# Optimization experiments

Measured on AMD Instinct MI355X. Metric: run time of the kernel, lower is better.

## Reference

```python
import jax, jax.numpy as jnp
import numpy as np

# ---- static synthetic forest: 64 complete binary trees, depth 9 (heap layout) ----
DEPTH = 9
N_TREES = 64
C = 8
M = 256
N_GEN = 8
NPT = 2 ** (DEPTH + 1) - 1          # 1023 nodes per tree
DIM = N_TREES * NPT                  # 65472 total nodes
_base = np.arange(N_TREES) * NPT

def _lvl_nodes(l):
    return (_base[:, None] + np.arange(2 ** l - 1, 2 ** (l + 1) - 1)[None, :]).reshape(-1)

LEVELS = []   # list of (parent_idx, child_idx) edge arrays, top level first
UPAR = []     # unique parents per level (== nodes of level l-1)
for _l in range(1, DEPTH + 1):
    _ch = np.arange(2 ** _l - 1, 2 ** (_l + 1) - 1)
    _pa = (_ch - 1) // 2
    LEVELS.append((jnp.asarray((_base[:, None] + _pa[None, :]).reshape(-1)),
                   jnp.asarray((_base[:, None] + _ch[None, :]).reshape(-1))))
    UPAR.append(jnp.asarray(_lvl_nodes(_l - 1)))
LEAVES = jnp.asarray(_lvl_nodes(DEPTH))
ROOTS = jnp.asarray(_base)
INTERNAL = jnp.asarray(np.concatenate([_lvl_nodes(l) for l in range(DEPTH)]))
TREES_IND = jnp.asarray(np.repeat(np.arange(N_TREES), NPT))
N_CH = 2.0  # every internal node has exactly 2 children -> segment mean = sum/2


def _forward(A, B, Pi, x):
    # softmax reparameterization (per generative head)
    sm_A = jax.nn.softmax(A, axis=0)          # (C,C,G), softmax over parent-state dim 0
    sm_B = jax.nn.softmax(B, axis=1)          # (C,M,G), softmax over symbols
    sm_Pi = jax.nn.softmax(Pi, axis=0)        # (C,G)

    # B[:, x] gathered per node, as (node, C, G)
    B_x = jnp.transpose(sm_B[:, x], (1, 0, 2))  # (DIM,C,G)

    # ---- reversed upward (leaves -> roots) ----
    beta = jnp.zeros((DIM, C, N_GEN), dtype=A.dtype)
    t_beta = jnp.zeros((DIM, C, N_GEN), dtype=A.dtype)
    b_leaf = sm_Pi[None, :, :] * B_x[LEAVES]                 # (L,C,G)
    beta = beta.at[LEAVES].set(b_leaf / b_leaf.sum(1, keepdims=True))
    for (pa, ch), upar in zip(reversed(LEVELS), reversed(UPAR)):
        beta_ch = beta[ch]                                   # (E,C,G)
        t_beta_ch = jnp.einsum('ijg,ejg->eig', sm_A, beta_ch)
        t_beta = t_beta + jax.ops.segment_sum(t_beta_ch, pa, num_segments=DIM) / N_CH
        beta_l = t_beta[upar] * B_x[upar]                    # (U,C,G)
        beta = beta.at[upar].set(beta_l / beta_l.sum(1, keepdims=True))

    # ---- reversed downward (roots -> leaves) ----
    eps = jnp.zeros((DIM, C, N_GEN), dtype=A.dtype)
    t_eps = jnp.zeros((DIM, C, C, N_GEN), dtype=A.dtype)
    eps = eps.at[ROOTS].set(beta[ROOTS])
    for pa, ch in LEVELS:
        # (E,Cpa,Cch,G)
        eps_joint = (eps[pa][:, :, None, :] * sm_A[None]
                     * beta[ch][:, None, :, :] / t_beta[pa][:, :, None, :])
        t_eps = t_eps + jax.ops.segment_sum(eps_joint, pa, num_segments=DIM) / N_CH
        eps = eps.at[ch].set(eps_joint.sum(1))

    # ---- log-likelihood ----
    lik = jnp.zeros((DIM, N_GEN), dtype=A.dtype)
    lik = lik.at[INTERNAL].add((t_eps[INTERNAL] * jnp.log(sm_A)[None]).sum((1, 2)))
    lik = lik + (eps * jnp.log(B_x)).sum(1)  # all_nodes == all nodes here
    lik = lik.at[LEAVES].add((eps[LEAVES] * jnp.log(sm_Pi)[None]).sum(1))
    ll = jax.ops.segment_sum(lik, TREES_IND, num_segments=N_TREES)  # (n_trees,G)
    return -ll


def setup_inputs() -> dict:
    key = jax.random.key(0)
    k1, k2, k3, k4 = jax.random.split(key, 4)
    A = jax.random.uniform(k1, (C, C, N_GEN), minval=-5.0, maxval=5.0)
    B = jax.random.uniform(k2, (C, M, N_GEN), minval=-5.0, maxval=5.0)
    Pi = jax.random.uniform(k3, (C, N_GEN), minval=-5.0, maxval=5.0)
    x = jax.random.randint(k4, (DIM,), 0, M)
    return {"A": A, "B": B, "Pi": Pi, "x": x}


def reference(A, B, Pi, x):
    return _forward(A, B, Pi, x)
```

## Files before the change

### kernel.cpp

```cpp
#include <hip/hip_runtime.h>
#include <hip/hip_bf16.h>

#define NTHREADS 256

namespace {
constexpr int C = 8;
constexpr int G = 8;
constexpr int M = 256;
constexpr int DEPTH = 9;
constexpr int NPT = 1023;
constexpr int NINT = 511;

__global__ __launch_bounds__(NTHREADS, 2)
void htmm_fused(const float* __restrict__ A, const float* __restrict__ Bm,
                const float* __restrict__ Pi, const int* __restrict__ x,
                float* __restrict__ out)
{
    __shared__ float beta[NPT][9];
    __shared__ float tbeta[NINT][9];
    __shared__ __hip_bfloat16 bx[NPT][C];
    __shared__ float smA[C][C];
    __shared__ float AlogA[C][C];
    __shared__ float smPi[C];
    __shared__ float logPi[C];
    __shared__ float den[C];
    __shared__ float part[C][32];
    __shared__ float red[NTHREADS / 64];

    const int tid  = threadIdx.x;
    const int tree = blockIdx.x >> 3;
    const int g    = blockIdx.x & 7;

    if (tid < C * C) {
        int i = tid >> 3, j = tid & 7;
        smA[i][j] = A[(i * C + j) * G + g];
    }
    {
        int i = tid >> 5, t = tid & 31;
        float s = 0.f;
        for (int m = t; m < M; m += 32)
            s += __expf(Bm[(i * M + m) * G + g]);
        part[i][t] = s;
    }
    __syncthreads();

    if (tid < C) {
        int j = tid;
        float mx = -1e30f;
        for (int i = 0; i < C; ++i) mx = fmaxf(mx, smA[i][j]);
        float s = 0.f;
        for (int i = 0; i < C; ++i) s += __expf(smA[i][j] - mx);
        float ls = __logf(s);
        float inv = 1.f / s;
        for (int i = 0; i < C; ++i) {
            float raw = smA[i][j];
            float v = __expf(raw - mx) * inv;
            smA[i][j]  = v;
            AlogA[i][j] = v * (raw - mx - ls);
        }
    } else if (tid < 2 * C) {
        int i = tid - C;
        float s = 0.f;
        for (int t = 0; t < 32; ++t) s += part[i][t];
        den[i] = s;
    } else if (tid == 2 * C) {
        float raw[C];
        float mx = -1e30f;
        for (int i = 0; i < C; ++i) { raw[i] = Pi[i * G + g]; mx = fmaxf(mx, raw[i]); }
        float s = 0.f;
        for (int i = 0; i < C; ++i) s += __expf(raw[i] - mx);
        float ls = __logf(s);
        float inv = 1.f / s;
        for (int i = 0; i < C; ++i) {
            smPi[i]  = __expf(raw[i] - mx) * inv;
            logPi[i] = raw[i] - mx - ls;
        }
    }
    __syncthreads();

    for (int n = tid; n < NPT; n += NTHREADS) {
        int xn = x[tree * NPT + n];
        #pragma unroll
        for (int i = 0; i < C; ++i) {
            float v = __expf(Bm[(i * M + xn) * G + g]) / den[i];
            bx[n][i] = __float2bfloat16(v);
        }
    }
    __syncthreads();

    for (int n0 = tid; n0 < 512; n0 += NTHREADS) {
        int n = NINT + n0;
        float b[C], s = 0.f;
        #pragma unroll
        for (int i = 0; i < C; ++i) { b[i] = smPi[i] * __bfloat162float(bx[n][i]); s += b[i]; }
        float inv = 1.f / s;
        #pragma unroll
        for (int i = 0; i < C; ++i) beta[n][i] = b[i] * inv;
    }
    __syncthreads();

    for (int l = DEPTH; l >= 1; --l) {
        const int P = 1 << (l - 1);
        const int basep = P - 1;
        for (int it = tid; it < P * C; it += NTHREADS) {
            int pr = it >> 3, i = it & 7;
            int p = basep + pr;
            int cl = 2 * p + 1;
            float tb = 0.f;
            #pragma unroll
            for (int j = 0; j < C; ++j)
                tb += smA[i][j] * (beta[cl][j] + beta[cl + 1][j]);
            tbeta[p][i] = 0.5f * tb;
        }
        __syncthreads();
        for (int pr = tid; pr < P; pr += NTHREADS) {
            int p = basep + pr;
            float t[C], s = 0.f;
            #pragma unroll
            for (int i = 0; i < C; ++i) {
                t[i] = tbeta[p][i] * __bfloat162float(bx[p][i]);
                s += t[i];
            }
            float inv = 1.f / s;
            #pragma unroll
            for (int i = 0; i < C; ++i) beta[p][i] = t[i] * inv;
        }
        __syncthreads();
    }

    float acc = 0.f;
    if (tid < C) acc += beta[0][tid] * __logf(__bfloat162float(bx[0][tid]));

    for (int l = 1; l <= DEPTH; ++l) {
        const int P = 1 << (l - 1);
        const int basep = P - 1;
        const int basec = 2 * P - 1;
        for (int it = tid; it < P * C; it += NTHREADS) {
            int pr = it >> 3, i = it & 7;
            int p = basep + pr;
            tbeta[p][i] = beta[p][i] / tbeta[p][i];
        }
        __syncthreads();
        const bool leaf = (l == DEPTH);
        for (int it = tid; it < 2 * P * C; it += NTHREADS) {
            int cr = it >> 3, j = it & 7;
            int ch = basec + cr;
            int p  = basep + (cr >> 1);
            float es = 0.f, ts = 0.f;
            #pragma unroll
            for (int i = 0; i < C; ++i) {
                float w = tbeta[p][i];
                es += w * smA[i][j];
                ts += w * AlogA[i][j];
            }
            float br = beta[ch][j];
            float ev = br * es;
            acc += 0.5f * br * ts + ev * __logf(__bfloat162float(bx[ch][j]));
            if (leaf) acc += ev * logPi[j];
            beta[ch][j] = ev;
        }
        __syncthreads();
    }

    #pragma unroll
    for (int off = 32; off >= 1; off >>= 1)
        acc += __shfl_down(acc, off);
    if ((tid & 63) == 0) red[tid >> 6] = acc;
    __syncthreads();
    if (tid == 0)
        out[tree * G + g] = -(red[0] + red[1] + red[2] + red[3]);
}
}

extern "C" void kernel_launch(void* const* d_in, const int* in_sizes, int n_in,
                              void* d_out, int out_size, void* d_ws, size_t ws_size,
                              hipStream_t stream) {
    const float* A  = (const float*)d_in[0];
    const float* Bm = (const float*)d_in[1];
    const float* Pi = (const float*)d_in[2];
    const int*   x  = (const int*)d_in[3];
    float* out = (float*)d_out;
    hipLaunchKernelGGL(htmm_fused, dim3(64 * 8), dim3(NTHREADS), 0, stream,
                       A, Bm, Pi, x, out);
}
```

Before: 89.57 us.

## Restructure tree passes into wave-local subtrees with full softmax tables

Rewrites the fused kernel so each wavefront owns whole subtrees for the bottom levels of the upward and downward passes. Ordering between levels there uses wave barriers instead of block-wide __syncthreads, and only the top six levels run on a single wave. It also builds full normalized B and log-B tables in shared memory with shuffle reductions, dropping the per-node bf16 gather and per-node logf. The cost is a larger shared-memory footprint and an idle phase for three of the four waves during the top-level work.

```diff
diff --git a/kernel.cpp b/kernel.cpp
--- a/kernel.cpp
+++ b/kernel.cpp
@@ -1,174 +1,185 @@
 #include <hip/hip_runtime.h>
-#include <hip/hip_bf16.h>
 
-#define NTHREADS 256
+#define NT 256
 
 namespace {
-constexpr int C = 8;
-constexpr int G = 8;
-constexpr int M = 256;
-constexpr int DEPTH = 9;
-constexpr int NPT = 1023;
-constexpr int NINT = 511;
+constexpr int C = 8, G = 8, M = 256, NPT = 1023, NINT = 511;
 
-__global__ __launch_bounds__(NTHREADS, 2)
-void htmm_fused(const float* __restrict__ A, const float* __restrict__ Bm,
-                const float* __restrict__ Pi, const int* __restrict__ x,
+__global__ __launch_bounds__(NT, 2)
+void htmm_fused(const float* __restrict__ Ag, const float* __restrict__ Bg,
+                const float* __restrict__ Pig, const int* __restrict__ xg,
                 float* __restrict__ out)
 {
+    __shared__ int   xs[NPT + 1];
+    __shared__ float smB[C][M + 1];
+    __shared__ float logB[C][M + 1];
     __shared__ float beta[NPT][9];
-    __shared__ float tbeta[NINT][9];
-    __shared__ __hip_bfloat16 bx[NPT][C];
-    __shared__ float smA[C][C];
-    __shared__ float AlogA[C][C];
-    __shared__ float smPi[C];
-    __shared__ float logPi[C];
-    __shared__ float den[C];
-    __shared__ float part[C][32];
-    __shared__ float red[NTHREADS / 64];
+    __shared__ float tbe[NINT][9];
+    __shared__ float smA_s[C][9];
+    __shared__ float alA_s[C][9];
+    __shared__ float pi_s[2][C];
+    __shared__ float red[4];
 
     const int tid  = threadIdx.x;
-    const int tree = blockIdx.x >> 3;
-    const int g    = blockIdx.x & 7;
+    const int wv   = tid >> 6;
+    const int lane = tid & 63;
+    const int s    = lane >> 3;
+    const int q    = lane & 7;
+    const int tree = blockIdx.x >> 3, g = blockIdx.x & 7;
 
-    if (tid < C * C) {
-        int i = tid >> 3, j = tid & 7;
-        smA[i][j] = A[(i * C + j) * G + g];
+    for (int n = tid; n < NPT; n += NT) xs[n] = xg[tree * NPT + n];
+
+    {
+        const int i  = 2 * wv + (lane >> 5);
+        const int c0 = lane & 31;
+        float raw[8], ex[8], ssum = 0.f;
+        #pragma unroll
+        for (int t = 0; t < 8; ++t) {
+            raw[t] = Bg[(i * M + c0 + 32 * t) * G + g];
+            ex[t]  = __expf(raw[t]);
+            ssum  += ex[t];
+        }
+        #pragma unroll
+        for (int m = 1; m <= 16; m <<= 1) ssum += __shfl_xor(ssum, m);
+        const float inv = 1.f / ssum, ls = __logf(ssum);
+        #pragma unroll
+        for (int t = 0; t < 8; ++t) {
+            smB[i][c0 + 32 * t]  = ex[t] * inv;
+            logB[i][c0 + 32 * t] = raw[t] - ls;
+        }
     }
-    {
-        int i = tid >> 5, t = tid & 31;
-        float s = 0.f;
-        for (int m = t; m < M; m += 32)
-            s += __expf(Bm[(i * M + m) * G + g]);
-        part[i][t] = s;
+    if (wv == 0) {
+        const float raw = Ag[(s * C + q) * G + g];
+        float e = __expf(raw), S = e;
+        #pragma unroll
+        for (int m = 8; m <= 32; m <<= 1) S += __shfl_xor(S, m);
+        const float v = e / S;
+        smA_s[s][q] = v;
+        alA_s[s][q] = v * (raw - __logf(S));
+    } else if (wv == 1 && lane < C) {
+        const float raw = Pig[lane * G + g];
+        float e = __expf(raw), S = e;
+        #pragma unroll
+        for (int m = 1; m <= 4; m <<= 1) S += __shfl_xor(S, m);
+        pi_s[0][lane] = e / S;
+        pi_s[1][lane] = raw - __logf(S);
     }
     __syncthreads();
 
-    if (tid < C) {
-        int j = tid;
-        float mx = -1e30f;
-        for (int i = 0; i < C; ++i) mx = fmaxf(mx, smA[i][j]);
-        float s = 0.f;
-        for (int i = 0; i < C; ++i) s += __expf(smA[i][j] - mx);
-        float ls = __logf(s);
-        float inv = 1.f / s;
-        for (int i = 0; i < C; ++i) {
-            float raw = smA[i][j];
-            float v = __expf(raw - mx) * inv;
-            smA[i][j]  = v;
-            AlogA[i][j] = v * (raw - mx - ls);
+    float Arow[8], Acol[8], ALc[8], piR[8];
+    #pragma unroll
+    for (int j = 0; j < 8; ++j) Arow[j] = smA_s[q][j];
+    #pragma unroll
+    for (int i = 0; i < 8; ++i) { Acol[i] = smA_s[i][q]; ALc[i] = alA_s[i][q]; piR[i] = pi_s[0][i]; }
+    const float logPi_q = pi_s[1][q];
+
+    float acc = 0.f;
+
+    auto upstep = [&](int p) {
+        const int cl = 2 * p + 1;
+        float tb = 0.f;
+        #pragma unroll
+        for (int j = 0; j < 8; ++j) tb += Arow[j] * (beta[cl][j] + beta[cl + 1][j]);
+        tb *= 0.5f;
+        tbe[p][q] = tb;
+        float u = tb * smB[q][xs[p]];
+        float S = u;
+        #pragma unroll
+        for (int m = 1; m <= 4; m <<= 1) S += __shfl_xor(S, m);
+        beta[p][q] = u / S;
+    };
+    auto wstep = [&](int p) {
+        tbe[p][q] = beta[p][q] / tbe[p][q];
+    };
+    auto dstep = [&](int ch, int p, bool leaf) {
+        float es = 0.f, ts = 0.f;
+        #pragma unroll
+        for (int i = 0; i < 8; ++i) {
+            const float w = tbe[p][i];
+            es += w * Acol[i];
+            ts += w * ALc[i];
         }
-    } else if (tid < 2 * C) {
-        int i = tid - C;
-        float s = 0.f;
-        for (int t = 0; t < 32; ++t) s += part[i][t];
-        den[i] = s;
-    } else if (tid == 2 * C) {
-        float raw[C];
-        float mx = -1e30f;
-        for (int i = 0; i < C; ++i) { raw[i] = Pi[i * G + g]; mx = fmaxf(mx, raw[i]); }
-        float s = 0.f;
-        for (int i = 0; i < C; ++i) s += __expf(raw[i] - mx);
-        float ls = __logf(s);
-        float inv = 1.f / s;
-        for (int i = 0; i < C; ++i) {
-            smPi[i]  = __expf(raw[i] - mx) * inv;
-            logPi[i] = raw[i] - mx - ls;
+        const float br = beta[ch][q];
+        const float ev = br * es;
+        acc += 0.5f * br * ts + ev * logB[q][xs[ch]];
+        if (leaf) acc += ev * logPi_q;
+        else      beta[ch][q] = ev;
+    };
+
+    #pragma unroll
+    for (int g2 = 0; g2 < 2; ++g2) {
+        const int k0 = 16 * wv + 8 * g2, k = k0 + s;
+        {
+            const int n  = 511 + 8 * k0 + lane;
+            const int xv = xs[n];
+            float u[8], S = 0.f;
+            #pragma unroll
+            for (int i = 0; i < 8; ++i) { u[i] = piR[i] * smB[i][xv]; S += u[i]; }
+            const float inv = 1.f / S;
+            #pragma unroll
+            for (int i = 0; i < 8; ++i) beta[n][i] = u[i] * inv;
+        }
+        __builtin_amdgcn_wave_barrier();
+        #pragma unroll
+        for (int m = 0; m < 4; ++m) upstep(255 + 4 * k + m);
+        __builtin_amdgcn_wave_barrier();
+        #pragma unroll
+        for (int m = 0; m < 2; ++m) upstep(127 + 2 * k + m);
+        __builtin_amdgcn_wave_barrier();
+        upstep(63 + k);
+        __builtin_amdgcn_wave_barrier();
+    }
+    __syncthreads();
+
+    if (wv == 0) {
+        for (int d = 5; d >= 0; --d) {
+            const int Pd = 1 << d, base = Pd - 1;
+            for (int r0 = 0; r0 < Pd; r0 += 8)
+                if (r0 + s < Pd) upstep(base + r0 + s);
+            __builtin_amdgcn_wave_barrier();
+        }
+        if (lane < 8) acc += beta[0][lane] * logB[lane][xs[0]];
+        for (int dc = 1; dc <= 6; ++dc) {
+            const int Pp = 1 << (dc - 1), basep = Pp - 1, basec = 2 * Pp - 1, NC = 2 * Pp;
+            for (int r0 = 0; r0 < Pp; r0 += 8)
+                if (r0 + s < Pp) wstep(basep + r0 + s);
+            __builtin_amdgcn_wave_barrier();
+            for (int r0 = 0; r0 < NC; r0 += 8)
+                if (r0 + s < NC) {
+                    const int cr = r0 + s;
+                    dstep(basec + cr, basep + (cr >> 1), false);
+                }
+            __builtin_amdgcn_wave_barrier();
         }
     }
     __syncthreads();
 
-    for (int n = tid; n < NPT; n += NTHREADS) {
-        int xn = x[tree * NPT + n];
+    #pragma unroll
+    for (int g2 = 0; g2 < 2; ++g2) {
+        const int k = 16 * wv + 8 * g2 + s;
+        wstep(63 + k);
+        __builtin_amdgcn_wave_barrier();
         #pragma unroll
-        for (int i = 0; i < C; ++i) {
-            float v = __expf(Bm[(i * M + xn) * G + g]) / den[i];
-            bx[n][i] = __float2bfloat16(v);
-        }
-    }
-    __syncthreads();
-
-    for (int n0 = tid; n0 < 512; n0 += NTHREADS) {
-        int n = NINT + n0;
-        float b[C], s = 0.f;
+        for (int m = 0; m < 2; ++m) dstep(127 + 2 * k + m, 63 + k, false);
+        __builtin_amdgcn_wave_barrier();
         #pragma unroll
-        for (int i = 0; i < C; ++i) { b[i] = smPi[i] * __bfloat162float(bx[n][i]); s += b[i]; }
-        float inv = 1.f / s;
+        for (int m = 0; m < 2; ++m) wstep(127 + 2 * k + m);
+        __builtin_amdgcn_wave_barrier();
         #pragma unroll
-        for (int i = 0; i < C; ++i) beta[n][i] = b[i] * inv;
-    }
-    __syncthreads();
-
-    for (int l = DEPTH; l >= 1; --l) {
-        const int P = 1 << (l - 1);
-        const int basep = P - 1;
-        for (int it = tid; it < P * C; it += NTHREADS) {
-            int pr = it >> 3, i = it & 7;
-            int p = basep + pr;
-            int cl = 2 * p + 1;
-            float tb = 0.f;
-            #pragma unroll
-            for (int j = 0; j < C; ++j)
-                tb += smA[i][j] * (beta[cl][j] + beta[cl + 1][j]);
-            tbeta[p][i] = 0.5f * tb;
-        }
-        __syncthreads();
-        for (int pr = tid; pr < P; pr += NTHREADS) {
-            int p = basep + pr;
-            float t[C], s = 0.f;
-            #pragma unroll
-            for (int i = 0; i < C; ++i) {
-                t[i] = tbeta[p][i] * __bfloat162float(bx[p][i]);
-                s += t[i];
-            }
-            float inv = 1.f / s;
-            #pragma unroll
-            for (int i = 0; i < C; ++i) beta[p][i] = t[i] * inv;
-        }
-        __syncthreads();
-    }
-
-    float acc = 0.f;
-    if (tid < C) acc += beta[0][tid] * __logf(__bfloat162float(bx[0][tid]));
-
-    for (int l = 1; l <= DEPTH; ++l) {
-        const int P = 1 << (l - 1);
-        const int basep = P - 1;
-        const int basec = 2 * P - 1;
-        for (int it = tid; it < P * C; it += NTHREADS) {
-            int pr = it >> 3, i = it & 7;
-            int p = basep + pr;
-            tbeta[p][i] = beta[p][i] / tbeta[p][i];
-        }
-        __syncthreads();
-        const bool leaf = (l == DEPTH);
-        for (int it = tid; it < 2 * P * C; it += NTHREADS) {
-            int cr = it >> 3, j = it & 7;
-            int ch = basec + cr;
-            int p  = basep + (cr >> 1);
-            float es = 0.f, ts = 0.f;
-            #pragma unroll
-            for (int i = 0; i < C; ++i) {
-                float w = tbeta[p][i];
-                es += w * smA[i][j];
-                ts += w * AlogA[i][j];
-            }
-            float br = beta[ch][j];
-            float ev = br * es;
-            acc += 0.5f * br * ts + ev * __logf(__bfloat162float(bx[ch][j]));
-            if (leaf) acc += ev * logPi[j];
-            beta[ch][j] = ev;
-        }
-        __syncthreads();
+        for (int m = 0; m < 4; ++m) dstep(255 + 4 * k + m, 127 + 2 * k + (m >> 1), false);
+        __builtin_amdgcn_wave_barrier();
+        #pragma unroll
+        for (int m = 0; m < 4; ++m) wstep(255 + 4 * k + m);
+        __builtin_amdgcn_wave_barrier();
+        #pragma unroll
+        for (int m = 0; m < 8; ++m) dstep(511 + 8 * k + m, 255 + 4 * k + (m >> 1), true);
     }
 
     #pragma unroll
-    for (int off = 32; off >= 1; off >>= 1)
-        acc += __shfl_down(acc, off);
-    if ((tid & 63) == 0) red[tid >> 6] = acc;
+    for (int m = 1; m <= 32; m <<= 1) acc += __shfl_xor(acc, m);
+    if (lane == 0) red[wv] = acc;
     __syncthreads();
-    if (tid == 0)
-        out[tree * G + g] = -(red[0] + red[1] + red[2] + red[3]);
+    if (tid == 0) out[blockIdx.x] = -(red[0] + red[1] + red[2] + red[3]);
 }
 }
 
@@ -179,7 +190,7 @@
     const float* Bm = (const float*)d_in[1];
     const float* Pi = (const float*)d_in[2];
     const int*   x  = (const int*)d_in[3];
-    float* out = (float*)d_out;
-    hipLaunchKernelGGL(htmm_fused, dim3(64 * 8), dim3(NTHREADS), 0, stream,
-                       A, Bm, Pi, x, out);
+    float* o = (float*)d_out;
+    hipLaunchKernelGGL(htmm_fused, dim3(64 * 8), dim3(NT), 0, stream,
+                       A, Bm, Pi, x, o);
 }
```

Result: faster. 76.02 us (-15.1%).
